# Performance work log

Hardware: AMD Instinct MI355X
Metric: run time of the kernel (lower is better)

Reference implementation:

```python
import jax, jax.numpy as jnp
import numpy as np

VQ_ALPHA = 0.5   # non-trainable vq_alpha weight, constant 0.5
BETA = 0.25      # commitment loss weight


def setup_inputs() -> dict:
    key = jax.random.key(0)
    k1, k2 = jax.random.split(key)
    x = jax.random.normal(k1, (16, 64, 64, 256), dtype=jnp.float32)
    # tf.keras RandomUniform default is U(-0.05, 0.05)
    dictionary = jax.random.uniform(k2, (256, 1024), dtype=jnp.float32,
                                    minval=-0.05, maxval=0.05)
    return {"x": x, "dictionary": dictionary}


def reference(x, dictionary):
    D, K = dictionary.shape  # embedding_dim, num_embeddings
    flat = x.reshape(-1, D)  # [N, D]

    # squared L2 distances: ||f||^2 + ||d||^2 - 2 f.d   -> [N, K]
    similarity = flat @ dictionary
    distances = (jnp.sum(flat * flat, axis=1, keepdims=True)
                 + jnp.sum(dictionary * dictionary, axis=0, keepdims=True)
                 - 2.0 * similarity)
    code_idx = jnp.argmin(distances, axis=1)  # [N]

    # one-hot @ dict^T is just a row gather of dict^T
    quantized = jnp.take(dictionary.T, code_idx, axis=0)  # [N, D]
    quantized = VQ_ALPHA * quantized
    q = quantized.reshape(x.shape)

    dictionary_loss = jnp.mean(jnp.square(jax.lax.stop_gradient(x) - q))
    commitment_loss = jnp.mean(jnp.square(x - jax.lax.stop_gradient(q)))
    loss = dictionary_loss + BETA * commitment_loss

    # straight-through estimator
    q_st = x + jax.lax.stop_gradient(q - x)
    return q_st, loss
```

## Files before the change

### kernel.cpp

```cpp
#include <hip/hip_runtime.h>


#define NROWS   65536
#define DIM     256
#define NCODE   1024
#define RPB     64
#define EPS_TIE 4e-3f

typedef _Float16 half8 __attribute__((ext_vector_type(8)));
typedef float    f32x4 __attribute__((ext_vector_type(4)));


__global__ void k_transpose(const float* __restrict__ dict, float* __restrict__ dictT) {
    int t = blockIdx.x * 256 + threadIdx.x;
#pragma unroll
    for (int i = 0; i < 4; ++i) {
        int e = i * 65536 + t;
        int d = e >> 10, k = e & 1023;
        dictT[k * DIM + d] = dict[e];
    }
}

__global__ void k_norms(const float* __restrict__ dict, float* __restrict__ dictnorm) {
    int k = blockIdx.x * 256 + threadIdx.x;
    float s = 0.f;
#pragma unroll 8
    for (int d = 0; d < DIM; ++d) {
        float v = dict[d * NCODE + k];
        s = fmaf(v, v, s);
    }
    dictnorm[k] = s;
}

__global__ void k_pack(const float* __restrict__ dict, unsigned short* __restrict__ packB) {
    int gid = blockIdx.x * 256 + threadIdx.x;
#pragma unroll
    for (int ii = 0; ii < 4; ++ii) {
        int o = ii * 65536 + gid;
        int j = o & 7, q = (o >> 3) & 3, n = (o >> 5) & 1023, kk = o >> 15;
        int d = kk * 32 + q * 8 + j;
        _Float16 h = (_Float16)dict[d * NCODE + n];
        packB[o] = *(unsigned short*)&h;
    }
}

__device__ __forceinline__ float np_pairwise_sq_128(const float* a, int stride) {
    float r[8];
#pragma unroll
    for (int j = 0; j < 8; ++j) {
        float v = a[j * stride];
        r[j] = __fmul_rn(v, v);
    }
    for (int i = 8; i < 128; i += 8) {
#pragma unroll
        for (int j = 0; j < 8; ++j) {
            float v = a[(i + j) * stride];
            r[j] = __fadd_rn(r[j], __fmul_rn(v, v));
        }
    }
    return __fadd_rn(__fadd_rn(__fadd_rn(r[0], r[1]), __fadd_rn(r[2], r[3])),
                     __fadd_rn(__fadd_rn(r[4], r[5]), __fadd_rn(r[6], r[7])));
}


__global__ __launch_bounds__(256, 4) void k_vq(
    const float* __restrict__ x, const float* __restrict__ dict,
    const float* __restrict__ dictT, const float* __restrict__ dictnorm,
    const unsigned short* __restrict__ packB,
    float* __restrict__ out, double* __restrict__ block_sums)
{
    __shared__ __align__(16) unsigned short bstage[8 * 2048];
    __shared__ float row_m1[RPB], row_m2[RPB];
    __shared__ int   row_k1[RPB], row_k2[RPB];
    __shared__ float red_d[256];
    __shared__ int   red_k[256];
    __shared__ float wred[4];
    __shared__ int   amb_list[RPB];
    __shared__ int   amb_cnt;

    const int tid  = threadIdx.x;
    const int ln   = tid & 63, wv = tid >> 6;
    const int l15  = ln & 15, q = ln >> 4;
    const int row0 = blockIdx.x * RPB;

    if (tid == 0) amb_cnt = 0;

    half8 afrag[8];
    {
        const float* ar = x + (size_t)(row0 + wv * 16 + l15) * DIM + q * 8;
#pragma unroll
        for (int kk = 0; kk < 8; ++kk) {
            const float4 p0 = *(const float4*)(ar + kk * 32);
            const float4 p1 = *(const float4*)(ar + kk * 32 + 4);
            half8 h;
            h[0] = (_Float16)p0.x; h[1] = (_Float16)p0.y; h[2] = (_Float16)p0.z; h[3] = (_Float16)p0.w;
            h[4] = (_Float16)p1.x; h[5] = (_Float16)p1.y; h[6] = (_Float16)p1.z; h[7] = (_Float16)p1.w;
            afrag[kk] = h;
        }
    }

    float m1[4], m2[4]; int j1[4], j2[4];
#pragma unroll
    for (int i = 0; i < 4; ++i) { m1[i] = 3.0e38f; m2[i] = 3.0e38f; j1[i] = 0x7fffffff; j2[i] = 0x7fffffff; }

    for (int cc = 0; cc < 16; ++cc) {
        const int c0 = cc * 64;
        __syncthreads();
        {
            const unsigned short* src = packB + (size_t)c0 * 32 + tid * 8;
            uint4 tmp[8];
#pragma unroll
            for (int kk = 0; kk < 8; ++kk) tmp[kk] = *(const uint4*)(src + (size_t)kk * 32768);
#pragma unroll
            for (int kk = 0; kk < 8; ++kk) *(uint4*)&bstage[kk * 2048 + tid * 8] = tmp[kk];
        }
        __syncthreads();

        float dn[4];
#pragma unroll
        for (int t = 0; t < 4; ++t) dn[t] = dictnorm[c0 + t * 16 + l15];

        const f32x4 zero = {0.f, 0.f, 0.f, 0.f};
        f32x4 acc[4];
#pragma unroll
        for (int t = 0; t < 4; ++t) acc[t] = zero;

#pragma unroll
        for (int kk = 0; kk < 8; ++kk) {
#pragma unroll
            for (int t = 0; t < 4; ++t) {
                const half8 b = *(const half8*)&bstage[kk * 2048 + (t * 16 + l15) * 32 + q * 8];
                acc[t] = __builtin_amdgcn_mfma_f32_16x16x32_f16(afrag[kk], b, acc[t], 0, 0, 0);
            }
        }

#pragma unroll
        for (int t = 0; t < 4; ++t) {
            const int k = c0 + t * 16 + l15;
#pragma unroll
            for (int i = 0; i < 4; ++i) {
                const float s = fmaf(-2.f, acc[t][i], dn[t]);
                if (s < m1[i])      { m2[i] = m1[i]; j2[i] = j1[i]; m1[i] = s; j1[i] = k; }
                else if (s < m2[i]) { m2[i] = s; j2[i] = k; }
            }
        }
    }

#pragma unroll
    for (int i = 0; i < 4; ++i) {
        float a1 = m1[i], a2 = m2[i]; int b1 = j1[i], b2 = j2[i];
#pragma unroll
        for (int sft = 1; sft < 16; sft <<= 1) {
            float o1 = __shfl_xor(a1, sft);
            float o2 = __shfl_xor(a2, sft);
            int   p1 = __shfl_xor(b1, sft);
            int   p2 = __shfl_xor(b2, sft);
            if (o1 < a1 || (o1 == a1 && p1 < b1)) {
                bool t = (a1 < o2) || (a1 == o2 && b1 < p2);
                a2 = t ? a1 : o2; b2 = t ? b1 : p2;
                a1 = o1; b1 = p1;
            } else {
                bool t = (o1 < a2) || (o1 == a2 && p1 < b2);
                a2 = t ? o1 : a2; b2 = t ? p1 : b2;
            }
        }
        if (l15 == 0) {
            const int r = wv * 16 + q * 4 + i;
            row_m1[r] = a1; row_m2[r] = a2; row_k1[r] = b1; row_k2[r] = b2;
        }
    }
    __syncthreads();

    if (tid < RPB && (row_m2[tid] - row_m1[tid]) < EPS_TIE) {
        int p = atomicAdd(&amb_cnt, 1);
        amb_list[p] = tid;
    }
    __syncthreads();
    const int namb = amb_cnt;

    for (int a = 0; a < namb; ++a) {
        const int r = amb_list[a];
        const float* xr = x + (size_t)(row0 + r) * DIM;
        const float nf = __fadd_rn(np_pairwise_sq_128(xr, 1), np_pairwise_sq_128(xr + 128, 1));
        float bd = 3.4e38f; int bk = 0x7fffffff;
#pragma unroll
        for (int i = 0; i < 4; ++i) {
            const int k = i * 256 + tid;
            float sim = 0.f, nd = 0.f;
            for (int d = 0; d < DIM; ++d) {
                const float dv = dict[(size_t)d * NCODE + k];
                const float fv = xr[d];
                sim = fmaf(fv, dv, sim);
                nd  = __fadd_rn(nd, __fmul_rn(dv, dv));
            }
            const float dist = __fsub_rn(__fadd_rn(nf, nd), __fmul_rn(2.f, sim));
            if (dist < bd) { bd = dist; bk = k; }
        }
        red_d[tid] = bd; red_k[tid] = bk;
        __syncthreads();
        for (int s = 128; s > 0; s >>= 1) {
            if (tid < s) {
                const float od = red_d[tid + s]; const int ok = red_k[tid + s];
                if (od < red_d[tid] || (od == red_d[tid] && ok < red_k[tid])) {
                    red_d[tid] = od; red_k[tid] = ok;
                }
            }
            __syncthreads();
        }
        if (tid == 0) row_k1[r] = red_k[0];
        __syncthreads();
    }

    float lsum = 0.f;
#pragma unroll 2
    for (int i = 0; i < 16; ++i) {
        const int e = i * 1024 + tid * 4;
        const int r = e >> 8, d0 = e & 255;
        const int kk = row_k1[r];
        const float4 dv = *(const float4*)&dictT[(size_t)kk * DIM + d0];
        const float4 xv = *(const float4*)&x[(size_t)row0 * DIM + e];
        float4 qv; qv.x = 0.5f * dv.x; qv.y = 0.5f * dv.y; qv.z = 0.5f * dv.z; qv.w = 0.5f * dv.w;
        float4 ov;
        ov.x = __fadd_rn(xv.x, __fsub_rn(qv.x, xv.x));
        ov.y = __fadd_rn(xv.y, __fsub_rn(qv.y, xv.y));
        ov.z = __fadd_rn(xv.z, __fsub_rn(qv.z, xv.z));
        ov.w = __fadd_rn(xv.w, __fsub_rn(qv.w, xv.w));
        const float e0 = __fsub_rn(xv.x, qv.x), e1 = __fsub_rn(xv.y, qv.y);
        const float e2 = __fsub_rn(xv.z, qv.z), e3 = __fsub_rn(xv.w, qv.w);
        lsum += e0 * e0 + e1 * e1 + e2 * e2 + e3 * e3;
        *(float4*)&out[(size_t)row0 * DIM + e] = ov;
    }

#pragma unroll
    for (int sft = 32; sft > 0; sft >>= 1) lsum += __shfl_down(lsum, sft, 64);
    if ((tid & 63) == 0) wred[tid >> 6] = lsum;
    __syncthreads();
    if (tid == 0)
        block_sums[blockIdx.x] = (double)((wred[0] + wred[1]) + (wred[2] + wred[3]));
}


__global__ void k_finalize(const double* __restrict__ block_sums, float* __restrict__ out_loss) {
    __shared__ double w[16];
    const int t = threadIdx.x;
    double v = block_sums[t];
#pragma unroll
    for (int sft = 32; sft > 0; sft >>= 1) v += __shfl_down(v, sft, 64);
    if ((t & 63) == 0) w[t >> 6] = v;
    __syncthreads();
    if (t == 0) {
        double tot = 0.0;
        for (int i = 0; i < 16; ++i) tot += w[i];
        out_loss[0] = (float)(1.25 * tot / (double)(NROWS * DIM));
    }
}


extern "C" void kernel_launch(void* const* d_in, const int* in_sizes, int n_in,
                              void* d_out, int out_size, void* d_ws, size_t ws_size,
                              hipStream_t stream) {
    (void)in_sizes; (void)n_in; (void)out_size; (void)ws_size;
    const float* x    = (const float*)d_in[0];
    const float* dict = (const float*)d_in[1];
    float* out = (float*)d_out;

    char* ws = (char*)d_ws;
    float*          dictT      = (float*)ws;
    float*          dictnorm   = (float*)(ws + 1048576);
    double*         block_sums = (double*)(ws + 1048576 + 4096);
    unsigned short* packB      = (unsigned short*)(ws + 1048576 + 4096 + 8192);

    k_transpose<<<256, 256, 0, stream>>>(dict, dictT);
    k_norms<<<4, 256, 0, stream>>>(dict, dictnorm);
    k_pack<<<256, 256, 0, stream>>>(dict, packB);
    k_vq<<<NROWS / RPB, 256, 0, stream>>>(x, dict, dictT, dictnorm, packB, out, block_sums);
    k_finalize<<<1, 1024, 0, stream>>>(block_sums, out + (size_t)NROWS * DIM);
}
```

Measured before the change: 307.0 us.

## Fuse prep kernels, double rows per wave, prefetch codebook tiles, swizzle LDS

Merges the transpose, norm and pack kernels into one prep launch, and the pack step now goes through a shared-memory tile so its writes are coalesced. The VQ kernel uses 128 threads, each wave covering 32 rows, so every B fragment read from LDS feeds two MFMAs. The next codebook chunk is prefetched into registers while the current one is used, and the LDS layout is swizzled to avoid bank conflicts. The top-2 tracking becomes branchless with med3/fmin and drops the second index. Costs are higher register pressure and fewer threads per block.

New measurement: 474.8 us. 1.55x slower.

```diff
diff --git a/kernel.cpp b/kernel.cpp
--- a/kernel.cpp
+++ b/kernel.cpp
@@ -10,51 +10,64 @@
 typedef _Float16 half8 __attribute__((ext_vector_type(8)));
 typedef float    f32x4 __attribute__((ext_vector_type(4)));
 
-
-__global__ void k_transpose(const float* __restrict__ dict, float* __restrict__ dictT) {
-    int t = blockIdx.x * 256 + threadIdx.x;
-#pragma unroll
-    for (int i = 0; i < 4; ++i) {
-        int e = i * 65536 + t;
-        int d = e >> 10, k = e & 1023;
-        dictT[k * DIM + d] = dict[e];
-    }
-}
-
-__global__ void k_norms(const float* __restrict__ dict, float* __restrict__ dictnorm) {
-    int k = blockIdx.x * 256 + threadIdx.x;
-    float s = 0.f;
+__global__ __launch_bounds__(256) void k_prep(const float* __restrict__ dict,
+                                              float* __restrict__ dictT,
+                                              float* __restrict__ dictnorm,
+                                              unsigned short* __restrict__ packB) {
+    const int b = blockIdx.x, tid = threadIdx.x;
+    if (b < 256) {
+        int t = b * 256 + tid;
+#pragma unroll
+        for (int i = 0; i < 4; ++i) {
+            int e = i * 65536 + t;
+            int d = e >> 10, k = e & 1023;
+            dictT[k * DIM + d] = dict[e];
+        }
+    } else if (b < 260) {
+        int k = (b - 256) * 256 + tid;
+        float s = 0.f;
 #pragma unroll 8
-    for (int d = 0; d < DIM; ++d) {
-        float v = dict[d * NCODE + k];
-        s = fmaf(v, v, s);
-    }
-    dictnorm[k] = s;
-}
-
-__global__ void k_pack(const float* __restrict__ dict, unsigned short* __restrict__ packB) {
-    int gid = blockIdx.x * 256 + threadIdx.x;
-#pragma unroll
-    for (int ii = 0; ii < 4; ++ii) {
-        int o = ii * 65536 + gid;
-        int j = o & 7, q = (o >> 3) & 3, n = (o >> 5) & 1023, kk = o >> 15;
-        int d = kk * 32 + q * 8 + j;
-        _Float16 h = (_Float16)dict[d * NCODE + n];
-        packB[o] = *(unsigned short*)&h;
-    }
-}
-
-__device__ __forceinline__ float np_pairwise_sq_128(const float* a, int stride) {
+        for (int d = 0; d < DIM; ++d) {
+            float v = dict[d * NCODE + k];
+            s = fmaf(v, v, s);
+        }
+        dictnorm[k] = s;
+    } else {
+        __shared__ float tile[32][257];
+        const int pb = b - 260;
+        const int kk = pb >> 2, kg = pb & 3;
+#pragma unroll
+        for (int dl = 0; dl < 32; ++dl)
+            tile[dl][tid] = dict[(kk * 32 + dl) * NCODE + kg * 256 + tid];
+        __syncthreads();
+        unsigned int* dst = (unsigned int*)(packB + (size_t)kk * 32768 + (size_t)(kg * 256 + tid) * 32);
+#pragma unroll
+        for (int q = 0; q < 4; ++q) {
+            unsigned int w[4];
+#pragma unroll
+            for (int p = 0; p < 4; ++p) {
+                _Float16 h0 = (_Float16)tile[q * 8 + p * 2 + 0][tid];
+                _Float16 h1 = (_Float16)tile[q * 8 + p * 2 + 1][tid];
+                unsigned short u0 = *(unsigned short*)&h0;
+                unsigned short u1 = *(unsigned short*)&h1;
+                w[p] = (unsigned int)u0 | ((unsigned int)u1 << 16);
+            }
+            *(uint4*)(dst + q * 4) = make_uint4(w[0], w[1], w[2], w[3]);
+        }
+    }
+}
+
+__device__ __forceinline__ float np_pairwise_sq_128(const float* a) {
     float r[8];
 #pragma unroll
     for (int j = 0; j < 8; ++j) {
-        float v = a[j * stride];
+        float v = a[j];
         r[j] = __fmul_rn(v, v);
     }
     for (int i = 8; i < 128; i += 8) {
 #pragma unroll
         for (int j = 0; j < 8; ++j) {
-            float v = a[(i + j) * stride];
+            float v = a[i + j];
             r[j] = __fadd_rn(r[j], __fmul_rn(v, v));
         }
     }
@@ -63,18 +76,18 @@
 }
 
 
-__global__ __launch_bounds__(256, 4) void k_vq(
+__global__ __launch_bounds__(128, 2) void k_vq(
     const float* __restrict__ x, const float* __restrict__ dict,
     const float* __restrict__ dictT, const float* __restrict__ dictnorm,
     const unsigned short* __restrict__ packB,
     float* __restrict__ out, double* __restrict__ block_sums)
 {
-    __shared__ __align__(16) unsigned short bstage[8 * 2048];
+    __shared__ __align__(16) uint4 bstage[2048];
     __shared__ float row_m1[RPB], row_m2[RPB];
-    __shared__ int   row_k1[RPB], row_k2[RPB];
-    __shared__ float red_d[256];
-    __shared__ int   red_k[256];
-    __shared__ float wred[4];
+    __shared__ int   row_k1[RPB];
+    __shared__ float red_d[128];
+    __shared__ int   red_k[128];
+    __shared__ float wred[2];
     __shared__ int   amb_list[RPB];
     __shared__ int   amb_cnt;
 
@@ -85,9 +98,10 @@
 
     if (tid == 0) amb_cnt = 0;
 
-    half8 afrag[8];
-    {
-        const float* ar = x + (size_t)(row0 + wv * 16 + l15) * DIM + q * 8;
+    half8 afrag[2][8];
+#pragma unroll
+    for (int rt = 0; rt < 2; ++rt) {
+        const float* ar = x + (size_t)(row0 + wv * 32 + rt * 16 + l15) * DIM + q * 8;
 #pragma unroll
         for (int kk = 0; kk < 8; ++kk) {
             const float4 p0 = *(const float4*)(ar + kk * 32);
@@ -95,78 +109,101 @@
             half8 h;
             h[0] = (_Float16)p0.x; h[1] = (_Float16)p0.y; h[2] = (_Float16)p0.z; h[3] = (_Float16)p0.w;
             h[4] = (_Float16)p1.x; h[5] = (_Float16)p1.y; h[6] = (_Float16)p1.z; h[7] = (_Float16)p1.w;
-            afrag[kk] = h;
-        }
-    }
-
-    float m1[4], m2[4]; int j1[4], j2[4];
-#pragma unroll
-    for (int i = 0; i < 4; ++i) { m1[i] = 3.0e38f; m2[i] = 3.0e38f; j1[i] = 0x7fffffff; j2[i] = 0x7fffffff; }
+            afrag[rt][kk] = h;
+        }
+    }
+
+    float m1[8], m2[8]; int j1[8];
+#pragma unroll
+    for (int s = 0; s < 8; ++s) { m1[s] = 3.0e38f; m2[s] = 3.0e38f; j1[s] = 0x7ffffff0; }
+
+    const uint4* pbu = (const uint4*)packB;
+    const int qw = tid & 3, nb = tid >> 2;
+
+    uint4 tmp[16];
+#pragma unroll
+    for (int kk = 0; kk < 8; ++kk)
+#pragma unroll
+        for (int h = 0; h < 2; ++h)
+            tmp[kk * 2 + h] = pbu[kk * 4096 + (nb + h * 32) * 4 + qw];
 
     for (int cc = 0; cc < 16; ++cc) {
+        __syncthreads();
+#pragma unroll
+        for (int kk = 0; kk < 8; ++kk)
+#pragma unroll
+            for (int h = 0; h < 2; ++h) {
+                const int n = nb + h * 32;
+                bstage[kk * 256 + n * 4 + ((qw + (n >> 2)) & 3)] = tmp[kk * 2 + h];
+            }
+        __syncthreads();
+
+        if (cc < 15) {
+            const int c1 = (cc + 1) * 64;
+#pragma unroll
+            for (int kk = 0; kk < 8; ++kk)
+#pragma unroll
+                for (int h = 0; h < 2; ++h)
+                    tmp[kk * 2 + h] = pbu[kk * 4096 + (c1 + nb + h * 32) * 4 + qw];
+        }
+
         const int c0 = cc * 64;
-        __syncthreads();
-        {
-            const unsigned short* src = packB + (size_t)c0 * 32 + tid * 8;
-            uint4 tmp[8];
-#pragma unroll
-            for (int kk = 0; kk < 8; ++kk) tmp[kk] = *(const uint4*)(src + (size_t)kk * 32768);
-#pragma unroll
-            for (int kk = 0; kk < 8; ++kk) *(uint4*)&bstage[kk * 2048 + tid * 8] = tmp[kk];
-        }
-        __syncthreads();
-
         float dn[4];
 #pragma unroll
         for (int t = 0; t < 4; ++t) dn[t] = dictnorm[c0 + t * 16 + l15];
 
         const f32x4 zero = {0.f, 0.f, 0.f, 0.f};
-        f32x4 acc[4];
-#pragma unroll
-        for (int t = 0; t < 4; ++t) acc[t] = zero;
+        f32x4 acc[2][4];
+#pragma unroll
+        for (int t = 0; t < 4; ++t) { acc[0][t] = zero; acc[1][t] = zero; }
 
 #pragma unroll
         for (int kk = 0; kk < 8; ++kk) {
 #pragma unroll
             for (int t = 0; t < 4; ++t) {
-                const half8 b = *(const half8*)&bstage[kk * 2048 + (t * 16 + l15) * 32 + q * 8];
-                acc[t] = __builtin_amdgcn_mfma_f32_16x16x32_f16(afrag[kk], b, acc[t], 0, 0, 0);
+                const int n = t * 16 + l15;
+                const half8 bf = *(const half8*)&bstage[kk * 256 + n * 4 + ((q + (n >> 2)) & 3)];
+                acc[0][t] = __builtin_amdgcn_mfma_f32_16x16x32_f16(afrag[0][kk], bf, acc[0][t], 0, 0, 0);
+                acc[1][t] = __builtin_amdgcn_mfma_f32_16x16x32_f16(afrag[1][kk], bf, acc[1][t], 0, 0, 0);
             }
         }
 
 #pragma unroll
         for (int t = 0; t < 4; ++t) {
-            const int k = c0 + t * 16 + l15;
-#pragma unroll
-            for (int i = 0; i < 4; ++i) {
-                const float s = fmaf(-2.f, acc[t][i], dn[t]);
-                if (s < m1[i])      { m2[i] = m1[i]; j2[i] = j1[i]; m1[i] = s; j1[i] = k; }
-                else if (s < m2[i]) { m2[i] = s; j2[i] = k; }
-            }
-        }
-    }
-
-#pragma unroll
-    for (int i = 0; i < 4; ++i) {
-        float a1 = m1[i], a2 = m2[i]; int b1 = j1[i], b2 = j2[i];
+            const int kb = c0 + t * 16;
+#pragma unroll
+            for (int rt = 0; rt < 2; ++rt)
+#pragma unroll
+                for (int i = 0; i < 4; ++i) {
+                    const int sl = rt * 4 + i;
+                    const float s = fmaf(-2.f, acc[rt][t][i], dn[t]);
+                    const bool c = s < m1[sl];
+                    j1[sl] = c ? kb : j1[sl];
+                    m2[sl] = __builtin_amdgcn_fmed3f(s, m1[sl], m2[sl]);
+                    m1[sl] = fminf(s, m1[sl]);
+                }
+        }
+    }
+
+#pragma unroll
+    for (int sl = 0; sl < 8; ++sl) {
+        float a1 = m1[sl], a2 = m2[sl];
+        int   b1 = j1[sl] + l15;
 #pragma unroll
         for (int sft = 1; sft < 16; sft <<= 1) {
-            float o1 = __shfl_xor(a1, sft);
-            float o2 = __shfl_xor(a2, sft);
-            int   p1 = __shfl_xor(b1, sft);
-            int   p2 = __shfl_xor(b2, sft);
+            const float o1 = __shfl_xor(a1, sft);
+            const float o2 = __shfl_xor(a2, sft);
+            const int   p1 = __shfl_xor(b1, sft);
             if (o1 < a1 || (o1 == a1 && p1 < b1)) {
-                bool t = (a1 < o2) || (a1 == o2 && b1 < p2);
-                a2 = t ? a1 : o2; b2 = t ? b1 : p2;
-                a1 = o1; b1 = p1;
+                a2 = fminf(a1, o2); a1 = o1; b1 = p1;
             } else {
-                bool t = (o1 < a2) || (o1 == a2 && p1 < b2);
-                a2 = t ? o1 : a2; b2 = t ? p1 : b2;
+                a2 = fminf(o1, a2);
             }
         }
         if (l15 == 0) {
-            const int r = wv * 16 + q * 4 + i;
-            row_m1[r] = a1; row_m2[r] = a2; row_k1[r] = b1; row_k2[r] = b2;
+            const int rt = sl >> 2, i = sl & 3;
+            const int r = wv * 32 + rt * 16 + q * 4 + i;
+            row_m1[r] = a1; row_m2[r] = a2; row_k1[r] = b1;
         }
     }
     __syncthreads();
@@ -181,11 +218,11 @@
     for (int a = 0; a < namb; ++a) {
         const int r = amb_list[a];
         const float* xr = x + (size_t)(row0 + r) * DIM;
-        const float nf = __fadd_rn(np_pairwise_sq_128(xr, 1), np_pairwise_sq_128(xr + 128, 1));
+        const float nf = __fadd_rn(np_pairwise_sq_128(xr), np_pairwise_sq_128(xr + 128));
         float bd = 3.4e38f; int bk = 0x7fffffff;
 #pragma unroll
-        for (int i = 0; i < 4; ++i) {
-            const int k = i * 256 + tid;
+        for (int i = 0; i < 8; ++i) {
+            const int k = i * 128 + tid;
             float sim = 0.f, nd = 0.f;
             for (int d = 0; d < DIM; ++d) {
                 const float dv = dict[(size_t)d * NCODE + k];
@@ -198,7 +235,7 @@
         }
         red_d[tid] = bd; red_k[tid] = bk;
         __syncthreads();
-        for (int s = 128; s > 0; s >>= 1) {
+        for (int s = 64; s > 0; s >>= 1) {
             if (tid < s) {
                 const float od = red_d[tid + s]; const int ok = red_k[tid + s];
                 if (od < red_d[tid] || (od == red_d[tid] && ok < red_k[tid])) {
@@ -212,9 +249,9 @@
     }
 
     float lsum = 0.f;
-#pragma unroll 2
-    for (int i = 0; i < 16; ++i) {
-        const int e = i * 1024 + tid * 4;
+#pragma unroll 4
+    for (int it = 0; it < 32; ++it) {
+        const int e = it * 512 + tid * 4;
         const int r = e >> 8, d0 = e & 255;
         const int kk = row_k1[r];
         const float4 dv = *(const float4*)&dictT[(size_t)kk * DIM + d0];
@@ -233,24 +270,23 @@
 
 #pragma unroll
     for (int sft = 32; sft > 0; sft >>= 1) lsum += __shfl_down(lsum, sft, 64);
-    if ((tid & 63) == 0) wred[tid >> 6] = lsum;
+    if (ln == 0) wred[wv] = lsum;
     __syncthreads();
     if (tid == 0)
-        block_sums[blockIdx.x] = (double)((wred[0] + wred[1]) + (wred[2] + wred[3]));
+        block_sums[blockIdx.x] = (double)(wred[0] + wred[1]);
 }
 
 
 __global__ void k_finalize(const double* __restrict__ block_sums, float* __restrict__ out_loss) {
-    __shared__ double w[16];
+    __shared__ double w[4];
     const int t = threadIdx.x;
-    double v = block_sums[t];
+    double v = block_sums[t] + block_sums[t + 256] + block_sums[t + 512] + block_sums[t + 768];
 #pragma unroll
     for (int sft = 32; sft > 0; sft >>= 1) v += __shfl_down(v, sft, 64);
     if ((t & 63) == 0) w[t >> 6] = v;
     __syncthreads();
     if (t == 0) {
-        double tot = 0.0;
-        for (int i = 0; i < 16; ++i) tot += w[i];
+        const double tot = (w[0] + w[1]) + (w[2] + w[3]);
         out_loss[0] = (float)(1.25 * tot / (double)(NROWS * DIM));
     }
 }
@@ -270,9 +306,7 @@
     double*         block_sums = (double*)(ws + 1048576 + 4096);
     unsigned short* packB      = (unsigned short*)(ws + 1048576 + 4096 + 8192);
 
-    k_transpose<<<256, 256, 0, stream>>>(dict, dictT);
-    k_norms<<<4, 256, 0, stream>>>(dict, dictnorm);
-    k_pack<<<256, 256, 0, stream>>>(dict, packB);
-    k_vq<<<NROWS / RPB, 256, 0, stream>>>(x, dict, dictT, dictnorm, packB, out, block_sums);
-    k_finalize<<<1, 1024, 0, stream>>>(block_sums, out + (size_t)NROWS * DIM);
-}
+    k_prep<<<292, 256, 0, stream>>>(dict, dictT, dictnorm, packB);
+    k_vq<<<NROWS / RPB, 128, 0, stream>>>(x, dict, dictT, dictnorm, packB, out, block_sums);
+    k_finalize<<<1, 256, 0, stream>>>(block_sums, out + (size_t)NROWS * DIM);
+}
```
